# Performance work log

Measured on AMD Instinct MI355X. Metric: run time of the kernel, lower is better.

The kernel has to match this reference:

```python
import jax, jax.numpy as jnp
import numpy as np

OUT, IN = 8192, 8192
GROUP = 128
N_GROUPS = IN // GROUP
BATCH = 64


def dequant_int4(packed, scales):
    # packed: [OUT, IN//2] int32 bytes in [0,256); two 4-bit codes per byte
    low = packed & 0xF            # first element of each pair
    high = (packed >> 4) & 0xF    # second element
    q = jnp.stack([low, high], axis=-1).reshape(OUT, IN)  # interleaved nibbles
    # symmetric grouped dequant: w = (q - 8) * scale, scale per [row, group]
    qg = q.reshape(OUT, N_GROUPS, GROUP).astype(scales.dtype)
    w = (qg - 8.0) * scales[:, :, None]
    return w.reshape(OUT, IN)


def setup_inputs() -> dict:
    key = jax.random.key(0)
    k1, k2, k3 = jax.random.split(key, 3)
    x = jax.random.normal(k1, (BATCH, IN), dtype=jnp.float32)
    packed = jax.random.randint(k2, (OUT, IN // 2), 0, 256, dtype=jnp.int32)
    scales = jax.random.uniform(k3, (OUT, N_GROUPS), dtype=jnp.float32)
    return {"x": x, "packed": packed, "scales": scales}


def reference(x, packed, scales):
    # Dequantize int4 weights then dense matmul (F.linear, no bias)
    w = dequant_int4(packed, scales)        # [OUT, IN]
    return jnp.einsum('bi,oi->bo', x, w)    # [BATCH, OUT]
```

## Files before the change

### kernel.cpp

```cpp
#include <hip/hip_runtime.h>
#include <hip/hip_bf16.h>
#include <stdint.h>

#define OUTN   8192
#define INN    8192
#define NGRP   64
#define BATCHN 64
#define BN     64
#define BK     128
#define KSPLIT 8
#define KCHUNK (INN / KSPLIT)
#define NITER  (KCHUNK / BK)
#define OSZ    (BATCHN * OUTN)

typedef __attribute__((ext_vector_type(8))) short bf16x8;
typedef __attribute__((ext_vector_type(4))) float f32x4;
typedef __attribute__((ext_vector_type(4))) unsigned int u32x4;

#define BARRIER_KEEP_VMEM() asm volatile("s_waitcnt lgkmcnt(0)\n\ts_barrier" ::: "memory")

__device__ __forceinline__ unsigned short f2bf(float f) {
  __hip_bfloat16 h = __float2bfloat16(f);
  return __builtin_bit_cast(unsigned short, h);
}
__device__ __forceinline__ float bf2f(unsigned short h) {
  unsigned int u = ((unsigned int)h) << 16;
  return __builtin_bit_cast(float, u);
}

__global__ void qlin_prep(const float* __restrict__ x, float* __restrict__ xsum) {
  const int b = blockIdx.x;
  const int t = threadIdx.x;
  const float* xrow = x + (size_t)b * INN + t * 32;
  float s = 0.0f;
#pragma unroll
  for (int i = 0; i < 8; ++i) {
    float4 v = *(const float4*)(xrow + i * 4);
    s += bf2f(f2bf(v.x)) + bf2f(f2bf(v.y)) + bf2f(f2bf(v.z)) + bf2f(f2bf(v.w));
  }
  __shared__ float part[256];
  part[t] = s;
  __syncthreads();
  if (t < NGRP) {
    float g = part[4 * t] + part[4 * t + 1] + part[4 * t + 2] + part[4 * t + 3];
    xsum[t * BATCHN + b] = g;
  }
}

__global__ void qlin_swz(const float* __restrict__ x, unsigned short* __restrict__ xswz) {
  const int idx = blockIdx.x * 256 + threadIdx.x;
  const int b  = idx >> 10;
  const int kc = idx & 1023;
  const float* p = x + (size_t)b * INN + kc * 8;
  float4 v0 = *(const float4*)p;
  float4 v1 = *(const float4*)(p + 4);
  u32x4 o;
  o.x = (unsigned)f2bf(v0.x) | ((unsigned)f2bf(v0.y) << 16);
  o.y = (unsigned)f2bf(v0.z) | ((unsigned)f2bf(v0.w) << 16);
  o.z = (unsigned)f2bf(v1.x) | ((unsigned)f2bf(v1.y) << 16);
  o.w = (unsigned)f2bf(v1.z) | ((unsigned)f2bf(v1.w) << 16);
  *(u32x4*)&xswz[(size_t)b * INN + kc * 8] = o;
}

#define PKS 17
#define XTS 136

__global__ __launch_bounds__(256, 4) void qlin_main(
    const int* __restrict__ packed, const float* __restrict__ scales,
    const unsigned short* __restrict__ xswz, const float* __restrict__ xsum,
    float* __restrict__ out, float* __restrict__ part) {
  const int bx    = blockIdx.x;
  const int ks    = bx & (KSPLIT - 1);
  const int ntile = bx >> 3;
  const int o0    = ntile * BN;
  const int g0    = ks * NITER;

  const int t    = threadIdx.x;
  const int lane = t & 63;
  const int w    = t >> 6;
  const int r    = lane & 15;
  const int q    = lane >> 4;
  const int orow = o0 + w * 16 + r;

  __shared__ __align__(16) unsigned int   pk_c[BN * PKS];
  __shared__ __align__(16) unsigned short xt[BATCHN * XTS];
  __shared__ __align__(16) float          xs[NITER][BATCHN];

#pragma unroll
  for (int i = 0; i < 2; ++i) {
    int v = t * 2 + i;
    xs[v >> 6][v & 63] = xsum[(g0 + (v >> 6)) * BATCHN + (v & 63)];
  }

  float4 sa = *(const float4*)&scales[(size_t)orow * NGRP + g0];
  float4 sb = *(const float4*)&scales[(size_t)orow * NGRP + g0 + 4];
  float sreg[8] = {sa.x, sa.y, sa.z, sa.w, sb.x, sb.y, sb.z, sb.w};

  int4  pkr[4];
  u32x4 xr4[4];
  const int prow = t >> 4, pcol = t & 15;
  const int xrow = t >> 2, xseg = t & 3;

  auto load_tile = [&](int i) {
    const int kk2 = ks * (KCHUNK / 2) + i * (BK / 2);
    const int* pbase = packed + (size_t)(o0 + prow) * (INN / 2) + kk2 + pcol * 4;
#pragma unroll
    for (int j = 0; j < 4; ++j)
      pkr[j] = *(const int4*)(pbase + (size_t)(16 * j) * (INN / 2));
    const unsigned short* xbase =
        xswz + (size_t)xrow * INN + ks * KCHUNK + i * BK + xseg * 32;
#pragma unroll
    for (int j = 0; j < 4; ++j)
      xr4[j] = *(const u32x4*)(xbase + j * 8);
  };

  auto store_tile = [&]() {
#pragma unroll
    for (int j = 0; j < 4; ++j) {
      unsigned int c = (unsigned)pkr[j].x | ((unsigned)pkr[j].y << 8) |
                       ((unsigned)pkr[j].z << 16) | ((unsigned)pkr[j].w << 24);
      pk_c[(prow + 16 * j) * PKS + pcol] = c;
    }
#pragma unroll
    for (int j = 0; j < 4; ++j)
      *(u32x4*)&xt[xrow * XTS + xseg * 32 + j * 8] = xr4[j];
  };

  f32x4 facc[4];
#pragma unroll
  for (int mt = 0; mt < 4; ++mt) facc[mt] = (f32x4){0.f, 0.f, 0.f, 0.f};

  load_tile(0);

  for (int i = 0; i < NITER; ++i) {
    BARRIER_KEEP_VMEM();
    store_tile();
    if (i + 1 < NITER) load_tile(i + 1);
    BARRIER_KEEP_VMEM();

    f32x4 gacc[4];
#pragma unroll
    for (int mt = 0; mt < 4; ++mt) gacc[mt] = (f32x4){0.f, 0.f, 0.f, 0.f};

#pragma unroll
    for (int kq = 0; kq < 4; ++kq) {
      bf16x8 af[4];
#pragma unroll
      for (int mt = 0; mt < 4; ++mt)
        af[mt] = *(const bf16x8*)&xt[(mt * 16 + r) * XTS + kq * 32 + q * 8];

      unsigned int c = pk_c[(w * 16 + r) * PKS + kq * 4 + q];
      u32x4 bw;
      bw.x = 0x43004300u | (c & 0xFu) | ((c & 0xF0u) << 12);
      bw.y = 0x43004300u | ((c >> 8) & 0xFu) | (((c >> 8) & 0xF0u) << 12);
      bw.z = 0x43004300u | ((c >> 16) & 0xFu) | (((c >> 16) & 0xF0u) << 12);
      bw.w = 0x43004300u | ((c >> 24) & 0xFu) | (((c >> 24) & 0xF0u) << 12);
      bf16x8 bfv = __builtin_bit_cast(bf16x8, bw);

#pragma unroll
      for (int mt = 0; mt < 4; ++mt)
        gacc[mt] = __builtin_amdgcn_mfma_f32_16x16x32_bf16(af[mt], bfv, gacc[mt], 0, 0, 0);
    }

    float sg = sreg[i];
#pragma unroll
    for (int mt = 0; mt < 4; ++mt) {
      f32x4 xv = *(const f32x4*)&xs[i][mt * 16 + q * 4];
#pragma unroll
      for (int rr = 0; rr < 4; ++rr)
        facc[mt][rr] += sg * (gacc[mt][rr] - 136.0f * xv[rr]);
    }
  }

  if (part) {
    float* pb = part + (size_t)ks * OSZ;
#pragma unroll
    for (int mt = 0; mt < 4; ++mt)
#pragma unroll
      for (int rr = 0; rr < 4; ++rr) {
        int m = mt * 16 + q * 4 + rr;
        pb[(size_t)m * OUTN + orow] = facc[mt][rr];
      }
  } else {
#pragma unroll
    for (int mt = 0; mt < 4; ++mt)
#pragma unroll
      for (int rr = 0; rr < 4; ++rr) {
        int m = mt * 16 + q * 4 + rr;
        atomicAdd(&out[(size_t)m * OUTN + orow], facc[mt][rr]);
      }
  }
}

__global__ void qlin_reduce(const float* __restrict__ part, float* __restrict__ out) {
  const size_t i = ((size_t)blockIdx.x * 256 + threadIdx.x) * 4;
  float4 s = *(const float4*)(part + i);
#pragma unroll
  for (int ks = 1; ks < KSPLIT; ++ks) {
    float4 v = *(const float4*)(part + (size_t)ks * OSZ + i);
    s.x += v.x; s.y += v.y; s.z += v.z; s.w += v.w;
  }
  *(float4*)(out + i) = s;
}

extern "C" void kernel_launch(void* const* d_in, const int* in_sizes, int n_in,
                              void* d_out, int out_size, void* d_ws, size_t ws_size,
                              hipStream_t stream) {
  const float* x      = (const float*)d_in[0];
  const int*   packed = (const int*)d_in[1];
  const float* scales = (const float*)d_in[2];
  float* out = (float*)d_out;

  char* ws = (char*)d_ws;
  float*          xsum = (float*)ws;
  unsigned short* xswz = (unsigned short*)(ws + 16384);
  const size_t part_need = 16384 + 1048576 + (size_t)KSPLIT * OSZ * sizeof(float);
  float* part = (ws_size >= part_need) ? (float*)(ws + 16384 + 1048576) : nullptr;

  qlin_prep<<<BATCHN, 256, 0, stream>>>(x, xsum);
  qlin_swz<<<(BATCHN * INN / 8) / 256, 256, 0, stream>>>(x, xswz);
  if (!part)
    hipMemsetAsync(d_out, 0, (size_t)out_size * sizeof(float), stream);
  qlin_main<<<(OUTN / BN) * KSPLIT, 256, 0, stream>>>(packed, scales, xswz, xsum, out, part);
  if (part)
    qlin_reduce<<<OSZ / 4 / 256, 256, 0, stream>>>(part, out);
}
```

Baseline: 209.3 us.

## Load packed weights directly into registers with double buffering, skip LDS staging

Each lane now loads its own packed int4 weight bytes straight from global memory into registers, with a two-deep register double buffer issued two iterations ahead, and dequantizes them in registers. This removes the LDS repacking store, the LDS read and one part of the barrier-bound traffic. The zero-point correction is moved out of the main loop and applied once at the end. The cost is higher register use, which may limit occupancy under the 256x4 launch bounds, and global loads that each pull in only a few useful bytes per 4-byte int.

```diff
diff --git a/kernel.cpp b/kernel.cpp
--- a/kernel.cpp
+++ b/kernel.cpp
@@ -62,7 +62,15 @@
   *(u32x4*)&xswz[(size_t)b * INN + kc * 8] = o;
 }
 
-#define PKS 17
+__device__ __forceinline__ bf16x8 dequant8(int4 c) {
+  u32x4 bw;
+  bw.x = 0x43004300u | ((unsigned)c.x & 0xFu) | (((unsigned)c.x & 0xF0u) << 12);
+  bw.y = 0x43004300u | ((unsigned)c.y & 0xFu) | (((unsigned)c.y & 0xF0u) << 12);
+  bw.z = 0x43004300u | ((unsigned)c.z & 0xFu) | (((unsigned)c.z & 0xF0u) << 12);
+  bw.w = 0x43004300u | ((unsigned)c.w & 0xFu) | (((unsigned)c.w & 0xF0u) << 12);
+  return __builtin_bit_cast(bf16x8, bw);
+}
+
 #define XTS 136
 
 __global__ __launch_bounds__(256, 4) void qlin_main(
@@ -82,7 +90,6 @@
   const int q    = lane >> 4;
   const int orow = o0 + w * 16 + r;
 
-  __shared__ __align__(16) unsigned int   pk_c[BN * PKS];
   __shared__ __align__(16) unsigned short xt[BATCHN * XTS];
   __shared__ __align__(16) float          xs[NITER][BATCHN];
 
@@ -96,17 +103,17 @@
   float4 sb = *(const float4*)&scales[(size_t)orow * NGRP + g0 + 4];
   float sreg[8] = {sa.x, sa.y, sa.z, sa.w, sb.x, sb.y, sb.z, sb.w};
 
-  int4  pkr[4];
+  const int* bptr = packed + (size_t)orow * (INN / 2) + ks * (KCHUNK / 2) + q * 4;
+  int4 bv[2][4];
+  auto loadB = [&](int g, int4* dst) {
+#pragma unroll
+    for (int s = 0; s < 4; ++s)
+      dst[s] = *(const int4*)(bptr + g * 64 + s * 16);
+  };
+
   u32x4 xr4[4];
-  const int prow = t >> 4, pcol = t & 15;
   const int xrow = t >> 2, xseg = t & 3;
-
-  auto load_tile = [&](int i) {
-    const int kk2 = ks * (KCHUNK / 2) + i * (BK / 2);
-    const int* pbase = packed + (size_t)(o0 + prow) * (INN / 2) + kk2 + pcol * 4;
-#pragma unroll
-    for (int j = 0; j < 4; ++j)
-      pkr[j] = *(const int4*)(pbase + (size_t)(16 * j) * (INN / 2));
+  auto loadX = [&](int i) {
     const unsigned short* xbase =
         xswz + (size_t)xrow * INN + ks * KCHUNK + i * BK + xseg * 32;
 #pragma unroll
@@ -114,28 +121,21 @@
       xr4[j] = *(const u32x4*)(xbase + j * 8);
   };
 
-  auto store_tile = [&]() {
-#pragma unroll
-    for (int j = 0; j < 4; ++j) {
-      unsigned int c = (unsigned)pkr[j].x | ((unsigned)pkr[j].y << 8) |
-                       ((unsigned)pkr[j].z << 16) | ((unsigned)pkr[j].w << 24);
-      pk_c[(prow + 16 * j) * PKS + pcol] = c;
-    }
+  loadX(0);
+  loadB(0, bv[0]);
+  loadB(1, bv[1]);
+
+  f32x4 facc[4];
+#pragma unroll
+  for (int mt = 0; mt < 4; ++mt) facc[mt] = (f32x4){0.f, 0.f, 0.f, 0.f};
+
+#pragma unroll
+  for (int i = 0; i < NITER; ++i) {
+    BARRIER_KEEP_VMEM();
 #pragma unroll
     for (int j = 0; j < 4; ++j)
       *(u32x4*)&xt[xrow * XTS + xseg * 32 + j * 8] = xr4[j];
-  };
-
-  f32x4 facc[4];
-#pragma unroll
-  for (int mt = 0; mt < 4; ++mt) facc[mt] = (f32x4){0.f, 0.f, 0.f, 0.f};
-
-  load_tile(0);
-
-  for (int i = 0; i < NITER; ++i) {
-    BARRIER_KEEP_VMEM();
-    store_tile();
-    if (i + 1 < NITER) load_tile(i + 1);
+    if (i + 1 < NITER) loadX(i + 1);
     BARRIER_KEEP_VMEM();
 
     f32x4 gacc[4];
@@ -148,27 +148,34 @@
 #pragma unroll
       for (int mt = 0; mt < 4; ++mt)
         af[mt] = *(const bf16x8*)&xt[(mt * 16 + r) * XTS + kq * 32 + q * 8];
-
-      unsigned int c = pk_c[(w * 16 + r) * PKS + kq * 4 + q];
-      u32x4 bw;
-      bw.x = 0x43004300u | (c & 0xFu) | ((c & 0xF0u) << 12);
-      bw.y = 0x43004300u | ((c >> 8) & 0xFu) | (((c >> 8) & 0xF0u) << 12);
-      bw.z = 0x43004300u | ((c >> 16) & 0xFu) | (((c >> 16) & 0xF0u) << 12);
-      bw.w = 0x43004300u | ((c >> 24) & 0xFu) | (((c >> 24) & 0xF0u) << 12);
-      bf16x8 bfv = __builtin_bit_cast(bf16x8, bw);
-
+      bf16x8 bfv = dequant8(bv[i & 1][kq]);
 #pragma unroll
       for (int mt = 0; mt < 4; ++mt)
         gacc[mt] = __builtin_amdgcn_mfma_f32_16x16x32_bf16(af[mt], bfv, gacc[mt], 0, 0, 0);
     }
 
+    if (i + 2 < NITER) loadB(i + 2, bv[i & 1]);
+
     float sg = sreg[i];
 #pragma unroll
+    for (int mt = 0; mt < 4; ++mt)
+#pragma unroll
+      for (int rr = 0; rr < 4; ++rr)
+        facc[mt][rr] += sg * gacc[mt][rr];
+  }
+
+  f32x4 corr[4];
+#pragma unroll
+  for (int mt = 0; mt < 4; ++mt) corr[mt] = (f32x4){0.f, 0.f, 0.f, 0.f};
+#pragma unroll
+  for (int g = 0; g < NITER; ++g) {
+    float sg = sreg[g];
+#pragma unroll
     for (int mt = 0; mt < 4; ++mt) {
-      f32x4 xv = *(const f32x4*)&xs[i][mt * 16 + q * 4];
+      f32x4 xv = *(const f32x4*)&xs[g][mt * 16 + q * 4];
 #pragma unroll
       for (int rr = 0; rr < 4; ++rr)
-        facc[mt][rr] += sg * (gacc[mt][rr] - 136.0f * xv[rr]);
+        corr[mt][rr] += sg * xv[rr];
     }
   }
 
@@ -179,7 +186,7 @@
 #pragma unroll
       for (int rr = 0; rr < 4; ++rr) {
         int m = mt * 16 + q * 4 + rr;
-        pb[(size_t)m * OUTN + orow] = facc[mt][rr];
+        pb[(size_t)m * OUTN + orow] = facc[mt][rr] - 136.0f * corr[mt][rr];
       }
   } else {
 #pragma unroll
@@ -187,7 +194,7 @@
 #pragma unroll
       for (int rr = 0; rr < 4; ++rr) {
         int m = mt * 16 + q * 4 + rr;
-        atomicAdd(&out[(size_t)m * OUTN + orow], facc[mt][rr]);
+        atomicAdd(&out[(size_t)m * OUTN + orow], facc[mt][rr] - 136.0f * corr[mt][rr]);
       }
   }
 }
```

Measured after the change: 210.5 us. Within noise of the previous version (+0.6%).
